# Kernel tuning notes

Measured on AMD Instinct MI355X. Metric: run time of the kernel, lower is better.

## Reference

```python
import jax, jax.numpy as jnp
import numpy as np
import math

B, WIN, C_IN, C_OUT = 8, 512, 38, 38
D_MODEL, N_HEADS, E_LAYERS, D_FF = 512, 8, 3, 512
EH = D_MODEL // N_HEADS
LN_EPS = 1e-3  # keras LayerNormalization default


def setup_inputs() -> dict:
    key = jax.random.key(0)
    ks = jax.random.split(key, 24)
    s = 0.02
    rn = lambda k, sh: jax.random.normal(k, sh, jnp.float32) * s
    L, d, H = E_LAYERS, D_MODEL, N_HEADS
    return {
        "x": jax.random.normal(ks[0], (B, WIN, C_IN), jnp.float32),
        "conv_k": rn(ks[1], (3, C_IN, d)),
        "Wq": rn(ks[2], (L, d, d)), "bq": jnp.zeros((L, d), jnp.float32),
        "Wk": rn(ks[3], (L, d, d)), "bk": jnp.zeros((L, d), jnp.float32),
        "Wv": rn(ks[4], (L, d, d)), "bv": jnp.zeros((L, d), jnp.float32),
        "Ws": rn(ks[5], (L, d, H)), "bs": jnp.zeros((L, H), jnp.float32),
        "Wo": rn(ks[6], (L, d, d)), "bo": jnp.zeros((L, d), jnp.float32),
        "W1": rn(ks[7], (L, d, D_FF)), "b1": jnp.zeros((L, D_FF), jnp.float32),
        "W2": rn(ks[8], (L, D_FF, d)), "b2": jnp.zeros((L, d), jnp.float32),
        "ln1_g": jnp.ones((L, d), jnp.float32), "ln1_b": jnp.zeros((L, d), jnp.float32),
        "ln2_g": jnp.ones((L, d), jnp.float32), "ln2_b": jnp.zeros((L, d), jnp.float32),
        "lnf_g": jnp.ones((d,), jnp.float32), "lnf_b": jnp.zeros((d,), jnp.float32),
        "Wp": rn(ks[9], (d, C_OUT)), "bp": jnp.zeros((C_OUT,), jnp.float32),
    }


def _layernorm(x, g, b):
    mu = jnp.mean(x, axis=-1, keepdims=True)
    var = jnp.mean((x - mu) ** 2, axis=-1, keepdims=True)
    return (x - mu) * jax.lax.rsqrt(var + LN_EPS) * g + b


def _pos_embedding():
    pos = jnp.arange(WIN, dtype=jnp.float32)[:, None]
    div = jnp.exp(jnp.arange(0, D_MODEL, 2, dtype=jnp.float32) * (-math.log(10000.0) / D_MODEL))
    # interleave sin at even idx, cos at odd idx
    return jnp.stack([jnp.sin(pos * div), jnp.cos(pos * div)], axis=-1).reshape(WIN, D_MODEL)


def reference(x, conv_k, Wq, bq, Wk, bk, Wv, bv, Ws, bs, Wo, bo,
              W1, b1, W2, b2, ln1_g, ln1_b, ln2_g, ln2_b, lnf_g, lnf_b, Wp, bp):
    # --- DataEmbedding: wrap-pad then Conv1D(k=3, valid), plus sinusoidal PE ---
    xp = jnp.concatenate([x[:, -1:], x, x[:, :1]], axis=1)
    h = jax.lax.conv_general_dilated(xp, conv_k, window_strides=(1,), padding='VALID',
                                     dimension_numbers=('NWC', 'WIO', 'NWC'))
    h = h + _pos_embedding()[None]

    idx = jnp.arange(WIN, dtype=jnp.float32)
    dist = jnp.abs(idx[:, None] - idx[None, :])
    scale = 1.0 / math.sqrt(EH)
    inv_sqrt_2pi = 1.0 / math.sqrt(2.0 * math.pi)

    series_l, prior_l, sigma_l = [], [], []
    for i in range(E_LAYERS):
        q = (h @ Wq[i] + bq[i]).reshape(B, WIN, N_HEADS, EH)
        k = (h @ Wk[i] + bk[i]).reshape(B, WIN, N_HEADS, EH)
        v = (h @ Wv[i] + bv[i]).reshape(B, WIN, N_HEADS, EH)
        sig = h @ Ws[i] + bs[i]

        scores = jnp.einsum('blhe,bshe->bhls', q, k)  # mask_flag=False in model
        series = jax.nn.softmax(scores * scale, axis=-1)  # [B, H, L, S]

        sg = jnp.transpose(sig, (0, 2, 1))               # [B, H, L]
        sg = jax.nn.sigmoid(sg * 5.0) + 1e-5
        sg = jnp.power(3.0, sg) - 1.0
        sg4 = jnp.broadcast_to(sg[..., None], (B, N_HEADS, WIN, WIN))
        prior = inv_sqrt_2pi / sg4 * jnp.exp(-(dist ** 2) / (2.0 * sg4 ** 2))

        attn_out = jnp.einsum('bhls,bshd->blhd', series, v).reshape(B, WIN, D_MODEL)
        h = _layernorm(h + attn_out @ Wo[i] + bo[i], ln1_g[i], ln1_b[i])
        y = jax.nn.gelu(h @ W1[i] + b1[i], approximate=False)
        y = y @ W2[i] + b2[i]
        h = _layernorm(h + y, ln2_g[i], ln2_b[i])

        series_l.append(series); prior_l.append(prior); sigma_l.append(sg4)

    h = _layernorm(h, lnf_g, lnf_b)
    out = h @ Wp + bp
    return (out, jnp.stack(series_l), jnp.stack(prior_l), jnp.stack(sigma_l))
```

## Files before the change

kernel.cpp:

```cpp
#include <hip/hip_runtime.h>
#include <math.h>


typedef unsigned short ushort;
typedef __attribute__((ext_vector_type(8))) ushort ushort8;
typedef __attribute__((ext_vector_type(4))) ushort ushort4v;
typedef __attribute__((ext_vector_type(8))) short short8;
typedef __attribute__((ext_vector_type(4))) float float4v;

__device__ inline ushort f2bf(float f) {
  union { float f; unsigned u; } v; v.f = f;
  return (ushort)((v.u + 0x7fffu + ((v.u >> 16) & 1u)) >> 16);
}

__device__ inline void gload16(const void* g, void* l) {
  __builtin_amdgcn_global_load_lds(
      (const __attribute__((address_space(1))) unsigned int*)g,
      (__attribute__((address_space(3))) unsigned int*)l, 16, 0, 0);
}

__global__ __launch_bounds__(512) void embed_kernel(const float* __restrict__ x,
                                                    const float* __restrict__ ck,
                                                    float* __restrict__ h,
                                                    ushort* __restrict__ hb) {
  int bt = blockIdx.x;
  int b = bt >> 9, t = bt & 511;
  int co = threadIdx.x;
  __shared__ float xs[3][38];
  if (co < 114) {
    int w = co / 38, ci = co - w * 38;
    int r = (t - 1 + w + 512) & 511;
    xs[w][ci] = x[((long)(b << 9) + r) * 38 + ci];
  }
  __syncthreads();
  float acc = 0.f;
#pragma unroll
  for (int w = 0; w < 3; ++w)
#pragma unroll
    for (int ci = 0; ci < 38; ++ci)
      acc = fmaf(xs[w][ci], ck[(w * 38 + ci) * 512 + co], acc);
  float div = expf((float)(co & ~1) * (-9.210340371976184f / 512.f));
  float ang = (float)t * div;
  float pe = (co & 1) ? cosf(ang) : sinf(ang);
  float o = acc + pe;
  h[(long)bt * 512 + co] = o;
  hb[(long)bt * 512 + co] = f2bf(o);
}

__global__ __launch_bounds__(256) void prep_kernel(
    const float* __restrict__ Wq, const float* __restrict__ Wk,
    const float* __restrict__ Wv, const float* __restrict__ Wo,
    const float* __restrict__ W1, const float* __restrict__ W2,
    ushort* __restrict__ wqkv, ushort* __restrict__ wo3,
    ushort* __restrict__ w13, ushort* __restrict__ w23) {
  int z = blockIdx.z;
  int ten = z / 3, l = z - ten * 3;
  const float* w;
  ushort* o;
  switch (ten) {
    case 0: w = Wq; o = wqkv + (long)l * 786432; break;
    case 1: w = Wk; o = wqkv + (long)l * 786432 + 262144; break;
    case 2: w = Wv; o = wqkv + (long)l * 786432 + 524288; break;
    case 3: w = Wo; o = wo3 + (long)l * 262144; break;
    case 4: w = W1; o = w13 + (long)l * 262144; break;
    default: w = W2; o = w23 + (long)l * 262144; break;
  }
  w += (long)l * 262144;
  int n = blockIdx.x * 256 + threadIdx.x;
  int c = blockIdx.y;
  ushort8 v;
#pragma unroll
  for (int i = 0; i < 8; ++i) v[i] = f2bf(w[(long)(c * 8 + i) * 512 + n]);
  *(ushort8*)&o[(long)n * 512 + c * 8] = v;
}

__global__ __launch_bounds__(512) void bw_kernel(const float* __restrict__ bq,
                                                 const float* __restrict__ bk,
                                                 const float* __restrict__ bv,
                                                 const float* __restrict__ Ws,
                                                 float* __restrict__ bqkv,
                                                 float* __restrict__ WsT) {
  int z = blockIdx.x, t = threadIdx.x;
  if (z < 3) {
    bqkv[z * 1536 + t] = bq[z * 512 + t];
    bqkv[z * 1536 + 512 + t] = bk[z * 512 + t];
    bqkv[z * 1536 + 1024 + t] = bv[z * 512 + t];
  } else {
    int l = z - 3;
#pragma unroll
    for (int hh = 0; hh < 8; ++hh)
      WsT[(long)l * 4096 + hh * 512 + t] = Ws[(long)l * 4096 + t * 8 + hh];
  }
}

template <bool GELU_, bool CBF16, bool VST>
__global__ __launch_bounds__(256) void gemm_bt(
    const ushort* __restrict__ A, int lda,
    const ushort* __restrict__ B, int ldb,
    const float* __restrict__ bias,
    void* __restrict__ Cv, int ldc, int K,
    ushort* __restrict__ vTout) {
  __shared__ ushort As[2][4096];
  __shared__ ushort Bs[2][2048];
  int t = threadIdx.x;
  int m0 = blockIdx.y * 128, n0 = blockIdx.x * 64;
  int w = t >> 6, lane = t & 63;
  int wr = (w >> 1) * 64, wc = (w & 1) * 32;
  int fm = lane & 15, q4 = lane >> 4;
  float4v acc[4][2];
#pragma unroll
  for (int i = 0; i < 4; ++i)
#pragma unroll
    for (int j = 0; j < 2; ++j) acc[i][j] = (float4v){0.f, 0.f, 0.f, 0.f};

  int kk = (lane & 3) * 8;
  const ushort* ga0 = &A[(long)(m0 + w * 32 + (lane >> 2)) * lda + kk];
  const ushort* ga1 = ga0 + (long)16 * lda;
  const ushort* gb = &B[(long)(n0 + w * 16 + (lane >> 2)) * ldb + kk];

  auto stage = [&](int bi) {
    gload16(ga0, &As[bi][w * 1024]);
    gload16(ga1, &As[bi][w * 1024 + 512]);
    gload16(gb, &Bs[bi][w * 512]);
    ga0 += 32; ga1 += 32; gb += 32;
  };
  auto compute = [&](int bi) {
    short8 a[4], bfr[2];
#pragma unroll
    for (int i = 0; i < 4; ++i)
      a[i] = *(const short8*)&As[bi][(wr + 16 * i + fm) * 32 + q4 * 8];
#pragma unroll
    for (int j = 0; j < 2; ++j)
      bfr[j] = *(const short8*)&Bs[bi][(wc + 16 * j + fm) * 32 + q4 * 8];
#pragma unroll
    for (int i = 0; i < 4; ++i)
#pragma unroll
      for (int j = 0; j < 2; ++j)
        acc[i][j] = __builtin_amdgcn_mfma_f32_16x16x32_bf16(a[i], bfr[j], acc[i][j], 0, 0, 0);
  };

  stage(0);
  __syncthreads();
#pragma unroll 1
  for (int k0 = 0; k0 < K; k0 += 64) {
    stage(1);
    compute(0);
    __syncthreads();
    if (k0 + 64 < K) stage(0);
    compute(1);
    __syncthreads();
  }

#pragma unroll
  for (int j = 0; j < 2; ++j) {
    int col = n0 + wc + 16 * j + fm;
    float bv = bias ? bias[col] : 0.f;
#pragma unroll
    for (int i = 0; i < 4; ++i) {
      int row0 = m0 + wr + 16 * i + q4 * 4;
      float vv[4];
#pragma unroll
      for (int r = 0; r < 4; ++r) {
        float v = acc[i][j][r] + bv;
        if (GELU_) v = 0.5f * v * (1.f + erff(v * 0.7071067811865476f));
        vv[r] = v;
        if (CBF16)
          ((ushort*)Cv)[(long)(row0 + r) * ldc + col] = f2bf(v);
        else
          ((float*)Cv)[(long)(row0 + r) * ldc + col] = v;
      }
      if (VST && n0 >= 1024) {
        int d = (col - 1024) & 63;
        int hh = (n0 - 1024) >> 6;
        int bb = row0 >> 9, s0 = row0 & 511;
        ushort4v pk;
#pragma unroll
        for (int r = 0; r < 4; ++r) pk[r] = f2bf(vv[r]);
        *(ushort4v*)&vTout[((long)(bb * 8 + hh) * 64 + d) * 512 + s0] = pk;
      }
    }
  }
}

__global__ __launch_bounds__(256, 2) void attn_fused(
    const ushort* __restrict__ qkv, const ushort* __restrict__ vT,
    const float* __restrict__ h, const float* __restrict__ WsT,
    const float* __restrict__ bsw,
    float* __restrict__ series, float* __restrict__ prior,
    float* __restrict__ sigma, ushort* __restrict__ t1b) {
  __shared__ ushort Ps[32 * 520];
  __shared__ float red[128];
  __shared__ float sgc[96];

  int t = threadIdx.x;
  int m0 = blockIdx.x * 32;
  int bh = blockIdx.y;
  int b = bh >> 3, hh = bh & 7;
  int w = t >> 6, lane = t & 63;
  int fm = lane & 15, q4 = lane >> 4;
  int wc = w * 128;
  long rowg = (long)b * 512;

  {
    int r = t >> 3, p = t & 7;
    const float* hrow = &h[(rowg + m0 + r) * 512 + p * 64];
    const float* wcol = &WsT[hh * 512 + p * 64];
    float s = 0.f;
#pragma unroll
    for (int i = 0; i < 16; ++i) {
      float4 hv = *(const float4*)&hrow[i * 4];
      float4 wv = *(const float4*)&wcol[i * 4];
      s += hv.x * wv.x + hv.y * wv.y + hv.z * wv.z + hv.w * wv.w;
    }
    s += __shfl_xor(s, 1); s += __shfl_xor(s, 2); s += __shfl_xor(s, 4);
    if (p == 0) {
      float xv = s + bsw[hh];
      float sig = 1.f / (1.f + __expf(-5.f * xv)) + 1e-5f;
      float sgv = expm1f(sig * 1.0986122886681098f);
      sgc[r * 3] = sgv;
      sgc[r * 3 + 1] = 0.3989422804014327f / sgv;
      sgc[r * 3 + 2] = 1.f / sgv;
    }
  }

  float4v acc[2][8];
#pragma unroll
  for (int i = 0; i < 2; ++i)
#pragma unroll
    for (int j = 0; j < 8; ++j) acc[i][j] = (float4v){0.f, 0.f, 0.f, 0.f};

  const ushort* qbase = &qkv[(rowg + m0) * 1536 + hh * 64];
  const ushort* kbase = &qkv[rowg * 1536 + 512 + hh * 64];
#pragma unroll
  for (int ks = 0; ks < 2; ++ks) {
    int ko = ks * 32 + q4 * 8;
    short8 a[2], bfr[8];
#pragma unroll
    for (int i = 0; i < 2; ++i)
      a[i] = *(const short8*)&qbase[(long)(16 * i + fm) * 1536 + ko];
#pragma unroll
    for (int j = 0; j < 8; ++j)
      bfr[j] = *(const short8*)&kbase[(long)(wc + 16 * j + fm) * 1536 + ko];
#pragma unroll
    for (int i = 0; i < 2; ++i)
#pragma unroll
      for (int j = 0; j < 8; ++j)
        acc[i][j] = __builtin_amdgcn_mfma_f32_16x16x32_bf16(a[i], bfr[j], acc[i][j], 0, 0, 0);
  }

#pragma unroll
  for (int i = 0; i < 2; ++i)
#pragma unroll
    for (int j = 0; j < 8; ++j)
#pragma unroll
      for (int r = 0; r < 4; ++r) acc[i][j][r] *= 0.125f;

  float mrow[2][4];
#pragma unroll
  for (int i = 0; i < 2; ++i)
#pragma unroll
    for (int r = 0; r < 4; ++r) {
      float m = acc[i][0][r];
#pragma unroll
      for (int j = 1; j < 8; ++j) m = fmaxf(m, acc[i][j][r]);
#pragma unroll
      for (int off = 1; off < 16; off <<= 1) m = fmaxf(m, __shfl_xor(m, off));
      mrow[i][r] = m;
    }
  if (fm == 0) {
#pragma unroll
    for (int i = 0; i < 2; ++i)
#pragma unroll
      for (int r = 0; r < 4; ++r)
        red[(16 * i + q4 * 4 + r) * 4 + w] = mrow[i][r];
  }
  __syncthreads();
#pragma unroll
  for (int i = 0; i < 2; ++i)
#pragma unroll
    for (int r = 0; r < 4; ++r) {
      const float* rp = &red[(16 * i + q4 * 4 + r) * 4];
      mrow[i][r] = fmaxf(fmaxf(rp[0], rp[1]), fmaxf(rp[2], rp[3]));
    }
  float lrow[2][4];
#pragma unroll
  for (int i = 0; i < 2; ++i)
#pragma unroll
    for (int r = 0; r < 4; ++r) {
      float s = 0.f;
#pragma unroll
      for (int j = 0; j < 8; ++j) {
        float e = __expf(acc[i][j][r] - mrow[i][r]);
        acc[i][j][r] = e;
        s += e;
      }
#pragma unroll
      for (int off = 1; off < 16; off <<= 1) s += __shfl_xor(s, off);
      lrow[i][r] = s;
    }
  __syncthreads();
  if (fm == 0) {
#pragma unroll
    for (int i = 0; i < 2; ++i)
#pragma unroll
      for (int r = 0; r < 4; ++r)
        red[(16 * i + q4 * 4 + r) * 4 + w] = lrow[i][r];
  }
  __syncthreads();
#pragma unroll
  for (int i = 0; i < 2; ++i)
#pragma unroll
    for (int r = 0; r < 4; ++r) {
      const float* rp = &red[(16 * i + q4 * 4 + r) * 4];
      lrow[i][r] = 1.f / (rp[0] + rp[1] + rp[2] + rp[3]);
    }

  float* serp = series + ((long)bh << 18);
#pragma unroll
  for (int i = 0; i < 2; ++i)
#pragma unroll
    for (int r = 0; r < 4; ++r) {
      int row = 16 * i + q4 * 4 + r;
      float inv = lrow[i][r];
#pragma unroll
      for (int j = 0; j < 8; ++j) {
        int col = wc + 16 * j + fm;
        float v = acc[i][j][r] * inv;
        __builtin_nontemporal_store(v, &serp[(long)(m0 + row) * 512 + col]);
        Ps[row * 520 + col] = f2bf(v);
      }
    }
  __syncthreads();

  float4v acc2[2] = {{0.f, 0.f, 0.f, 0.f}, {0.f, 0.f, 0.f, 0.f}};
  int wn = w * 16;
  const ushort* vbase = &vT[((long)bh * 64 + wn + fm) * 512];
#pragma unroll
  for (int c = 0; c < 8; ++c) {
#pragma unroll
    for (int ks = 0; ks < 2; ++ks) {
      int ko = ks * 32 + q4 * 8;
      short8 b2 = *(const short8*)&vbase[c * 64 + ko];
#pragma unroll
      for (int i = 0; i < 2; ++i) {
        short8 a2 = *(const short8*)&Ps[(16 * i + fm) * 520 + c * 64 + ko];
        acc2[i] = __builtin_amdgcn_mfma_f32_16x16x32_bf16(a2, b2, acc2[i], 0, 0, 0);
      }
    }
  }
#pragma unroll
  for (int i = 0; i < 2; ++i)
#pragma unroll
    for (int r = 0; r < 4; ++r)
      t1b[(rowg + m0 + 16 * i + q4 * 4 + r) * 512 + hh * 64 + wn + fm] =
          f2bf(acc2[i][r]);

  float* prip = prior + ((long)bh << 18);
  float* sigp = sigma + ((long)bh << 18);
  for (int it = t; it < 4096; it += 256) {
    int row = it >> 7;
    int c4 = (it & 127) << 2;
    float sgv = sgc[row * 3], inv = sgc[row * 3 + 1], rinv = sgc[row * 3 + 2];
    float ig = (float)(m0 + row);
    float4v pv, sv;
#pragma unroll
    for (int e = 0; e < 4; ++e) {
      float dd = ig - (float)(c4 + e);
      float rr = dd * rinv;
      pv[e] = inv * __expf(-0.5f * rr * rr);
      sv[e] = sgv;
    }
    __builtin_nontemporal_store(pv, (float4v*)&prip[(long)(m0 + row) * 512 + c4]);
    __builtin_nontemporal_store(sv, (float4v*)&sigp[(long)(m0 + row) * 512 + c4]);
  }
}

__global__ __launch_bounds__(256) void ln_kernel(const float* __restrict__ x,
                                                 const float* __restrict__ delta,
                                                 const float* __restrict__ g,
                                                 const float* __restrict__ bb,
                                                 float* __restrict__ out,
                                                 ushort* __restrict__ hb) {
  long row = blockIdx.x;
  int tid = threadIdx.x;
  int c = tid * 2;
  float2 xv = *(const float2*)&x[row * 512 + c];
  if (delta) {
    float2 dv = *(const float2*)&delta[row * 512 + c];
    xv.x += dv.x; xv.y += dv.y;
  }
  float s = xv.x + xv.y;
  float q = xv.x * xv.x + xv.y * xv.y;
#pragma unroll
  for (int off = 1; off < 64; off <<= 1) {
    s += __shfl_xor(s, off);
    q += __shfl_xor(q, off);
  }
  __shared__ float red[8];
  int wid = tid >> 6;
  if ((tid & 63) == 0) { red[wid] = s; red[wid + 4] = q; }
  __syncthreads();
  float S = red[0] + red[1] + red[2] + red[3];
  float Q = red[4] + red[5] + red[6] + red[7];
  float mean = S * (1.f / 512.f);
  float var = Q * (1.f / 512.f) - mean * mean;
  float rstd = rsqrtf(var + 1e-3f);
  float2 o;
  o.x = (xv.x - mean) * rstd * g[c] + bb[c];
  o.y = (xv.y - mean) * rstd * g[c + 1] + bb[c + 1];
  *(float2*)&out[row * 512 + c] = o;
  if (hb) {
    unsigned pk = ((unsigned)f2bf(o.y) << 16) | (unsigned)f2bf(o.x);
    ((unsigned*)hb)[row * 256 + tid] = pk;
  }
}

__global__ __launch_bounds__(256) void proj_ln(const float* __restrict__ A,
                                               const float* __restrict__ g,
                                               const float* __restrict__ bb,
                                               const float* __restrict__ W,
                                               const float* __restrict__ bp,
                                               float* __restrict__ C) {
  long row = (long)blockIdx.x * 4 + (threadIdx.x >> 6);
  int lane = threadIdx.x & 63;
  int k0 = lane * 8;
  float xv[8];
  {
    float4 x0 = *(const float4*)&A[row * 512 + k0];
    float4 x1 = *(const float4*)&A[row * 512 + k0 + 4];
    xv[0] = x0.x; xv[1] = x0.y; xv[2] = x0.z; xv[3] = x0.w;
    xv[4] = x1.x; xv[5] = x1.y; xv[6] = x1.z; xv[7] = x1.w;
  }
  float s = 0.f, q = 0.f;
#pragma unroll
  for (int e = 0; e < 8; ++e) { s += xv[e]; q += xv[e] * xv[e]; }
#pragma unroll
  for (int off = 1; off < 64; off <<= 1) {
    s += __shfl_xor(s, off);
    q += __shfl_xor(q, off);
  }
  float mean = s * (1.f / 512.f);
  float var = q * (1.f / 512.f) - mean * mean;
  float rstd = rsqrtf(var + 1e-3f);
  float acc[38];
#pragma unroll
  for (int j = 0; j < 38; ++j) acc[j] = 0.f;
#pragma unroll
  for (int e = 0; e < 8; ++e) {
    float xn = (xv[e] - mean) * rstd * g[k0 + e] + bb[k0 + e];
    const float* wr = &W[(long)(k0 + e) * 38];
#pragma unroll
    for (int j = 0; j < 38; ++j) acc[j] = fmaf(xn, wr[j], acc[j]);
  }
#pragma unroll
  for (int j = 0; j < 38; ++j)
#pragma unroll
    for (int off = 32; off; off >>= 1) acc[j] += __shfl_xor(acc[j], off);
  if (lane == 0) {
#pragma unroll
    for (int j = 0; j < 38; ++j) C[row * 38 + j] = acc[j] + bp[j];
  }
}

extern "C" void kernel_launch(void* const* d_in, const int* in_sizes, int n_in,
                              void* d_out, int out_size, void* d_ws, size_t ws_size,
                              hipStream_t stream) {
  (void)in_sizes; (void)n_in; (void)out_size; (void)ws_size;
  const float* x    = (const float*)d_in[0];
  const float* ck   = (const float*)d_in[1];
  const float* Wq   = (const float*)d_in[2];
  const float* bq   = (const float*)d_in[3];
  const float* Wk   = (const float*)d_in[4];
  const float* bk   = (const float*)d_in[5];
  const float* Wv   = (const float*)d_in[6];
  const float* bv   = (const float*)d_in[7];
  const float* Wsw  = (const float*)d_in[8];
  const float* bsw  = (const float*)d_in[9];
  const float* Wo   = (const float*)d_in[10];
  const float* bo   = (const float*)d_in[11];
  const float* W1   = (const float*)d_in[12];
  const float* b1   = (const float*)d_in[13];
  const float* W2   = (const float*)d_in[14];
  const float* b2   = (const float*)d_in[15];
  const float* ln1g = (const float*)d_in[16];
  const float* ln1b = (const float*)d_in[17];
  const float* ln2g = (const float*)d_in[18];
  const float* ln2b = (const float*)d_in[19];
  const float* lnfg = (const float*)d_in[20];
  const float* lnfb = (const float*)d_in[21];
  const float* Wp   = (const float*)d_in[22];
  const float* bp   = (const float*)d_in[23];
  float* out = (float*)d_out;

  float* h    = (float*)d_ws;
  float* t1   = h + 2097152;
  float* t2   = t1 + 2097152;
  float* wst  = t2 + 2097152;
  float* bqkv = wst + 32768;
  ushort* qkv  = (ushort*)(bqkv + 4608);
  ushort* wqkv = qkv + 6291456;
  ushort* wo3  = wqkv + 2359296;
  ushort* w13  = wo3 + 786432;
  ushort* w23  = w13 + 786432;
  ushort* t1b = (ushort*)t1;
  ushort* hb  = (ushort*)(t1 + 1048576);
  ushort* vT  = (ushort*)t2;

  float* series0 = out + 155648;
  float* prior0  = out + 50487296;
  float* sigma0  = out + 100818944;

  dim3 gPrep(2, 64, 18);
  prep_kernel<<<gPrep, 256, 0, stream>>>(Wq, Wk, Wv, Wo, W1, W2,
                                         wqkv, wo3, w13, w23);
  bw_kernel<<<6, 512, 0, stream>>>(bq, bk, bv, Wsw, bqkv, wst);

  embed_kernel<<<4096, 512, 0, stream>>>(x, ck, h, hb);

  dim3 gQKV(24, 32, 1);
  dim3 gFull(8, 32, 1);
  dim3 gAttn(16, 64, 1);

  for (int l = 0; l < 3; ++l) {
    float* ser = series0 + (long)l * 16777216;
    float* pri = prior0  + (long)l * 16777216;
    float* sgm = sigma0  + (long)l * 16777216;

    gemm_bt<false, true, true><<<gQKV, 256, 0, stream>>>(
        hb, 512, wqkv + (long)l * 786432, 512, bqkv + l * 1536, qkv, 1536, 512, vT);
    attn_fused<<<gAttn, 256, 0, stream>>>(qkv, vT, h, wst + (long)l * 4096,
                                          bsw + (long)l * 8, ser, pri, sgm, t1b);
    gemm_bt<false, false, false><<<gFull, 256, 0, stream>>>(
        t1b, 512, wo3 + (long)l * 262144, 512, bo + (long)l * 512, t2, 512, 512, nullptr);
    ln_kernel<<<4096, 256, 0, stream>>>(h, t2, ln1g + l * 512, ln1b + l * 512, h, hb);
    gemm_bt<true, true, false><<<gFull, 256, 0, stream>>>(
        hb, 512, w13 + (long)l * 262144, 512, b1 + (long)l * 512, t1b, 512, 512, nullptr);
    gemm_bt<false, false, false><<<gFull, 256, 0, stream>>>(
        t1b, 512, w23 + (long)l * 262144, 512, b2 + (long)l * 512, t2, 512, 512, nullptr);
    ln_kernel<<<4096, 256, 0, stream>>>(h, t2, ln2g + l * 512, ln2b + l * 512, h, hb);
  }

  proj_ln<<<1024, 256, 0, stream>>>(h, lnfg, lnfb, Wp, bp, out);
}
```

Before: 1.012 ms.

## Fuse residual+LayerNorm into output GEMMs and shrink GEMM tiles to 64x64

Adds a gemmln kernel in which each block computes a full 16x512 row strip of the Wo and W2 projections. It then adds bias and the residual and applies LayerNorm in the epilogue, writing both the fp32 and bf16 hidden states. This removes the separate ln_kernel launches and the fp32 round trip through t2. It also shrinks the generic gemm_bt tile from 128x64 to 64x64, doubling the grid for more parallelism on the QKV and FF1 GEMMs. The trade-off is that the fused kernel has only 256 blocks, each staging a whole 512-wide B slice per K step, and it reads resid from h while writing h in place.

Result: no change. 1.021 ms (+0.9%).

```diff
diff --git a/kernel.cpp b/kernel.cpp
--- a/kernel.cpp
+++ b/kernel.cpp
@@ -100,40 +100,38 @@
     const float* __restrict__ bias,
     void* __restrict__ Cv, int ldc, int K,
     ushort* __restrict__ vTout) {
-  __shared__ ushort As[2][4096];
+  __shared__ ushort As[2][2048];
   __shared__ ushort Bs[2][2048];
   int t = threadIdx.x;
-  int m0 = blockIdx.y * 128, n0 = blockIdx.x * 64;
+  int m0 = blockIdx.y * 64, n0 = blockIdx.x * 64;
   int w = t >> 6, lane = t & 63;
-  int wr = (w >> 1) * 64, wc = (w & 1) * 32;
+  int wr = (w >> 1) * 32, wc = (w & 1) * 32;
   int fm = lane & 15, q4 = lane >> 4;
-  float4v acc[4][2];
-#pragma unroll
-  for (int i = 0; i < 4; ++i)
+  float4v acc[2][2];
+#pragma unroll
+  for (int i = 0; i < 2; ++i)
 #pragma unroll
     for (int j = 0; j < 2; ++j) acc[i][j] = (float4v){0.f, 0.f, 0.f, 0.f};
 
   int kk = (lane & 3) * 8;
-  const ushort* ga0 = &A[(long)(m0 + w * 32 + (lane >> 2)) * lda + kk];
-  const ushort* ga1 = ga0 + (long)16 * lda;
+  const ushort* ga = &A[(long)(m0 + w * 16 + (lane >> 2)) * lda + kk];
   const ushort* gb = &B[(long)(n0 + w * 16 + (lane >> 2)) * ldb + kk];
 
   auto stage = [&](int bi) {
-    gload16(ga0, &As[bi][w * 1024]);
-    gload16(ga1, &As[bi][w * 1024 + 512]);
+    gload16(ga, &As[bi][w * 512]);
     gload16(gb, &Bs[bi][w * 512]);
-    ga0 += 32; ga1 += 32; gb += 32;
+    ga += 32; gb += 32;
   };
   auto compute = [&](int bi) {
-    short8 a[4], bfr[2];
-#pragma unroll
-    for (int i = 0; i < 4; ++i)
+    short8 a[2], bfr[2];
+#pragma unroll
+    for (int i = 0; i < 2; ++i)
       a[i] = *(const short8*)&As[bi][(wr + 16 * i + fm) * 32 + q4 * 8];
 #pragma unroll
     for (int j = 0; j < 2; ++j)
       bfr[j] = *(const short8*)&Bs[bi][(wc + 16 * j + fm) * 32 + q4 * 8];
 #pragma unroll
-    for (int i = 0; i < 4; ++i)
+    for (int i = 0; i < 2; ++i)
 #pragma unroll
       for (int j = 0; j < 2; ++j)
         acc[i][j] = __builtin_amdgcn_mfma_f32_16x16x32_bf16(a[i], bfr[j], acc[i][j], 0, 0, 0);
@@ -156,7 +154,7 @@
     int col = n0 + wc + 16 * j + fm;
     float bv = bias ? bias[col] : 0.f;
 #pragma unroll
-    for (int i = 0; i < 4; ++i) {
+    for (int i = 0; i < 2; ++i) {
       int row0 = m0 + wr + 16 * i + q4 * 4;
       float vv[4];
 #pragma unroll
@@ -182,6 +180,107 @@
   }
 }
 
+__global__ __launch_bounds__(256) void gemmln(
+    const ushort* __restrict__ A,
+    const ushort* __restrict__ B,
+    const float* __restrict__ bias,
+    const float* __restrict__ resid,
+    const float* __restrict__ g, const float* __restrict__ bb,
+    float* __restrict__ hout, ushort* __restrict__ hbout) {
+  __shared__ ushort As[2][512];
+  __shared__ ushort Bs[2][16384];
+  __shared__ float red[16][8];
+  int t = threadIdx.x;
+  int m0 = blockIdx.x * 16;
+  int w = t >> 6, lane = t & 63;
+  int fm = lane & 15, q4 = lane >> 4;
+
+  const ushort* ga = &A[(long)(m0 + (lane >> 2)) * 512 + (lane & 3) * 8];
+  const ushort* gb = &B[(long)(w * 128 + (lane >> 2)) * 512 + (lane & 3) * 8];
+
+  auto stage = [&](int bi) {
+    if (w == 0) gload16(ga, &As[bi][0]);
+    ga += 32;
+#pragma unroll
+    for (int c = 0; c < 8; ++c)
+      gload16(gb + (long)c * 16 * 512, &Bs[bi][(w * 128 + c * 16) * 32]);
+    gb += 32;
+  };
+
+  float4v acc[8];
+#pragma unroll
+  for (int j = 0; j < 8; ++j) acc[j] = (float4v){0.f, 0.f, 0.f, 0.f};
+
+  auto compute = [&](int bi) {
+    short8 a = *(const short8*)&As[bi][fm * 32 + q4 * 8];
+#pragma unroll
+    for (int j = 0; j < 8; ++j) {
+      short8 bfr = *(const short8*)&Bs[bi][(w * 128 + j * 16 + fm) * 32 + q4 * 8];
+      acc[j] = __builtin_amdgcn_mfma_f32_16x16x32_bf16(a, bfr, acc[j], 0, 0, 0);
+    }
+  };
+
+  stage(0);
+  __syncthreads();
+#pragma unroll 1
+  for (int k0 = 0; k0 < 512; k0 += 64) {
+    stage(1);
+    compute(0);
+    __syncthreads();
+    if (k0 + 64 < 512) stage(0);
+    compute(1);
+    __syncthreads();
+  }
+
+  float vv[8][4];
+  float sum[4] = {0.f, 0.f, 0.f, 0.f}, sq[4] = {0.f, 0.f, 0.f, 0.f};
+#pragma unroll
+  for (int j = 0; j < 8; ++j) {
+    int col = w * 128 + j * 16 + fm;
+    float bvv = bias[col];
+#pragma unroll
+    for (int r = 0; r < 4; ++r) {
+      int row = q4 * 4 + r;
+      float v = acc[j][r] + bvv + resid[(long)(m0 + row) * 512 + col];
+      vv[j][r] = v;
+      sum[r] += v;
+      sq[r] += v * v;
+    }
+  }
+#pragma unroll
+  for (int r = 0; r < 4; ++r) {
+#pragma unroll
+    for (int off = 1; off < 16; off <<= 1) {
+      sum[r] += __shfl_xor(sum[r], off);
+      sq[r] += __shfl_xor(sq[r], off);
+    }
+  }
+  if (fm == 0) {
+#pragma unroll
+    for (int r = 0; r < 4; ++r) {
+      red[q4 * 4 + r][w * 2] = sum[r];
+      red[q4 * 4 + r][w * 2 + 1] = sq[r];
+    }
+  }
+  __syncthreads();
+#pragma unroll
+  for (int r = 0; r < 4; ++r) {
+    int row = q4 * 4 + r;
+    float S = red[row][0] + red[row][2] + red[row][4] + red[row][6];
+    float Q = red[row][1] + red[row][3] + red[row][5] + red[row][7];
+    float mean = S * (1.f / 512.f);
+    float var = Q * (1.f / 512.f) - mean * mean;
+    float rstd = rsqrtf(var + 1e-3f);
+#pragma unroll
+    for (int j = 0; j < 8; ++j) {
+      int col = w * 128 + j * 16 + fm;
+      float xn = (vv[j][r] - mean) * rstd * g[col] + bb[col];
+      hout[(long)(m0 + row) * 512 + col] = xn;
+      hbout[(long)(m0 + row) * 512 + col] = f2bf(xn);
+    }
+  }
+}
+
 __global__ __launch_bounds__(256, 2) void attn_fused(
     const ushort* __restrict__ qkv, const ushort* __restrict__ vT,
     const float* __restrict__ h, const float* __restrict__ WsT,
@@ -372,46 +471,6 @@
     }
     __builtin_nontemporal_store(pv, (float4v*)&prip[(long)(m0 + row) * 512 + c4]);
     __builtin_nontemporal_store(sv, (float4v*)&sigp[(long)(m0 + row) * 512 + c4]);
-  }
-}
-
-__global__ __launch_bounds__(256) void ln_kernel(const float* __restrict__ x,
-                                                 const float* __restrict__ delta,
-                                                 const float* __restrict__ g,
-                                                 const float* __restrict__ bb,
-                                                 float* __restrict__ out,
-                                                 ushort* __restrict__ hb) {
-  long row = blockIdx.x;
-  int tid = threadIdx.x;
-  int c = tid * 2;
-  float2 xv = *(const float2*)&x[row * 512 + c];
-  if (delta) {
-    float2 dv = *(const float2*)&delta[row * 512 + c];
-    xv.x += dv.x; xv.y += dv.y;
-  }
-  float s = xv.x + xv.y;
-  float q = xv.x * xv.x + xv.y * xv.y;
-#pragma unroll
-  for (int off = 1; off < 64; off <<= 1) {
-    s += __shfl_xor(s, off);
-    q += __shfl_xor(q, off);
-  }
-  __shared__ float red[8];
-  int wid = tid >> 6;
-  if ((tid & 63) == 0) { red[wid] = s; red[wid + 4] = q; }
-  __syncthreads();
-  float S = red[0] + red[1] + red[2] + red[3];
-  float Q = red[4] + red[5] + red[6] + red[7];
-  float mean = S * (1.f / 512.f);
-  float var = Q * (1.f / 512.f) - mean * mean;
-  float rstd = rsqrtf(var + 1e-3f);
-  float2 o;
-  o.x = (xv.x - mean) * rstd * g[c] + bb[c];
-  o.y = (xv.y - mean) * rstd * g[c + 1] + bb[c + 1];
-  *(float2*)&out[row * 512 + c] = o;
-  if (hb) {
-    unsigned pk = ((unsigned)f2bf(o.y) << 16) | (unsigned)f2bf(o.x);
-    ((unsigned*)hb)[row * 256 + tid] = pk;
   }
 }
 
@@ -517,8 +576,8 @@
 
   embed_kernel<<<4096, 512, 0, stream>>>(x, ck, h, hb);
 
-  dim3 gQKV(24, 32, 1);
-  dim3 gFull(8, 32, 1);
+  dim3 gQKV(24, 64, 1);
+  dim3 gFF(8, 64, 1);
   dim3 gAttn(16, 64, 1);
 
   for (int l = 0; l < 3; ++l) {
@@ -530,14 +589,16 @@
         hb, 512, wqkv + (long)l * 786432, 512, bqkv + l * 1536, qkv, 1536, 512, vT);
     attn_fused<<<gAttn, 256, 0, stream>>>(qkv, vT, h, wst + (long)l * 4096,
                                           bsw + (long)l * 8, ser, pri, sgm, t1b);
-    gemm_bt<false, false, false><<<gFull, 256, 0, stream>>>(
-        t1b, 512, wo3 + (long)l * 262144, 512, bo + (long)l * 512, t2, 512, 512, nullptr);
-    ln_kernel<<<4096, 256, 0, stream>>>(h, t2, ln1g + l * 512, ln1b + l * 512, h, hb);
-    gemm_bt<true, true, false><<<gFull, 256, 0, stream>>>(
+    gemmln<<<256, 256, 0, stream>>>(t1b, wo3 + (long)l * 262144,
+                                    bo + (long)l * 512, h,
+                                    ln1g + (long)l * 512, ln1b + (long)l * 512,
+                                    h, hb);
+    gemm_bt<true, true, false><<<gFF, 256, 0, stream>>>(
         hb, 512, w13 + (long)l * 262144, 512, b1 + (long)l * 512, t1b, 512, 512, nullptr);
-    gemm_bt<false, false, false><<<gFull, 256, 0, stream>>>(
-        t1b, 512, w23 + (long)l * 262144, 512, b2 + (long)l * 512, t2, 512, 512, nullptr);
-    ln_kernel<<<4096, 256, 0, stream>>>(h, t2, ln2g + l * 512, ln2b + l * 512, h, hb);
+    gemmln<<<256, 256, 0, stream>>>(t1b, w23 + (long)l * 262144,
+                                    b2 + (long)l * 512, h,
+                                    ln2g + (long)l * 512, ln2b + (long)l * 512,
+                                    h, hb);
   }
 
   proj_ln<<<1024, 256, 0, stream>>>(h, lnfg, lnfb, Wp, bp, out);
```
